# Kernel tuning notes

Hardware: AMD Instinct MI355X
Metric: run time of the kernel (lower is better)

Reference implementation:

```python
import jax, jax.numpy as jnp
import numpy as np

F = 32        # num_fields
V = 1000      # per-field vocab (field_dims[i])
D = 64        # embed_dim
B = 8192      # batch
P = F * (F - 1) // 2   # 496 pairs
IN = F * D + P          # 2544 MLP input dim
H1, H2, OUT = 1024, 512, 1000


def setup_inputs() -> dict:
    key = jax.random.key(0)
    ks = jax.random.split(key, 8)
    x = jax.random.randint(ks[0], (B, F), 0, V)
    emb_tables = jax.random.normal(ks[1], (F, V, D), dtype=jnp.float32) * 0.05
    W1 = jax.random.normal(ks[2], (IN, H1), dtype=jnp.float32) * (1.0 / np.sqrt(IN))
    b1 = jnp.zeros((H1,), dtype=jnp.float32)
    W2 = jax.random.normal(ks[3], (H1, H2), dtype=jnp.float32) * (1.0 / np.sqrt(H1))
    b2 = jnp.zeros((H2,), dtype=jnp.float32)
    W3 = jax.random.normal(ks[4], (H2, OUT), dtype=jnp.float32) * (1.0 / np.sqrt(H2))
    b3 = jnp.zeros((OUT,), dtype=jnp.float32)
    return {"x": x, "emb_tables": emb_tables, "W1": W1, "b1": b1,
            "W2": W2, "b2": b2, "W3": W3, "b3": b3}


def reference(x, emb_tables, W1, b1, W2, b2, W3, b3):
    # Per-field embedding lookup: e[b, f] = emb_tables[f, x[b, f]]  -> (B, F, D)
    e = emb_tables[jnp.arange(F)[None, :], x]
    # All pairwise inner products via one batched gram matrix, then triu gather
    gram = jnp.einsum('bid,bjd->bij', e, e)            # (B, F, F)
    iu, ju = jnp.triu_indices(F, k=1)
    cross = gram[:, iu, ju]                             # (B, P)
    h = jnp.concatenate([e.reshape(B, F * D), cross], axis=1)  # (B, IN)
    # MLP (dropout is identity in eval mode)
    h = jax.nn.relu(h @ W1 + b1)
    h = jax.nn.relu(h @ W2 + b2)
    logits = h @ W3 + b3
    return jax.nn.sigmoid(logits)
```

## Files before the change

kernel.cpp:

```cpp
#include <hip/hip_runtime.h>
#include <hip/hip_bf16.h>
#include <cmath>

#define F_   32
#define V_   1000
#define D_   64
#define B_   8192
#define IN_RAW  2544
#define IN_PAD  2560
#define H1_  1024
#define H2_  512
#define OUT_RAW 1000
#define OUT_PAD 1024

typedef __attribute__((ext_vector_type(4))) float f32x4;
typedef __attribute__((ext_vector_type(8))) __bf16 bf16x8;

typedef const __attribute__((address_space(1))) void* gptr_t;
typedef __attribute__((address_space(3))) void* lptr_t;

__device__ __forceinline__ void gload_lds16(const void* g, void* l) {
  __builtin_amdgcn_global_load_lds((gptr_t)g, (lptr_t)l, 16, 0, 0);
}

#define MF(a, b, c) __builtin_amdgcn_mfma_f32_16x16x32_bf16((a), (b), (c), 0, 0, 0)
#define SBAR asm volatile("s_barrier" ::: "memory")
#define WAITV(n) asm volatile("s_waitcnt vmcnt(" #n ")" ::: "memory")

__global__ __launch_bounds__(256)
void prep_kernel(const int* __restrict__ x, const float* __restrict__ emb,
                 const float* __restrict__ W1, const float* __restrict__ W2,
                 const float* __restrict__ W3,
                 __hip_bfloat16* __restrict__ h, __hip_bfloat16* __restrict__ w1t,
                 __hip_bfloat16* __restrict__ w2t, __hip_bfloat16* __restrict__ w3t)
{
  __shared__ __align__(16) char smem[16384];
  const int bid = blockIdx.x;
  const int tid = threadIdx.x;

  if (bid < 3584) {
    const float* W; __hip_bfloat16* Wt; int K, N, Kpad, kb, nb;
    if (bid < 2560)      { W = W1; Wt = w1t; K = IN_RAW; N = H1_;     Kpad = IN_PAD; kb = bid % 80; nb = bid / 80; }
    else if (bid < 3072) { int r = bid - 2560; W = W2; Wt = w2t; K = H1_; N = H2_;   Kpad = H1_;   kb = r % 32;  nb = r / 32; }
    else                 { int r = bid - 3072; W = W3; Wt = w3t; K = H2_; N = OUT_RAW; Kpad = H2_; kb = r % 16;  nb = r / 16; }
    float (*t)[33] = (float(*)[33])smem;
    const int k0 = kb * 32, n0 = nb * 32;
    const int tx = tid & 31, ty = tid >> 5;
#pragma unroll
    for (int i = 0; i < 4; ++i) {
      int r = ty + i * 8;
      int k = k0 + r, n = n0 + tx;
      t[r][tx] = (k < K && n < N) ? W[(size_t)k * N + n] : 0.f;
    }
    __syncthreads();
#pragma unroll
    for (int i = 0; i < 4; ++i) {
      int r = ty + i * 8;
      Wt[(size_t)(n0 + r) * Kpad + (k0 + tx)] = __float2bfloat16(t[tx][r]);
    }
  } else {
    __hip_bfloat16 (*e4)[2048] = (__hip_bfloat16(*)[2048])smem;
    const int wid  = tid >> 6;
    const int lane = tid & 63;
    const int b = (bid - 3584) * 4 + wid;
    const int* xb = x + b * F_;
    const size_t hrow = (size_t)b * IN_PAD;

#pragma unroll
    for (int it = 0; it < 8; ++it) {
      const int r = it * 4 + (lane >> 4);
      const int d = (lane & 15) * 4;
      const int idx = xb[r];
      const float4 v = *reinterpret_cast<const float4*>(
          &emb[((size_t)r * V_ + idx) * D_ + d]);
      __hip_bfloat16 tb[4];
      tb[0] = __float2bfloat16(v.x); tb[1] = __float2bfloat16(v.y);
      tb[2] = __float2bfloat16(v.z); tb[3] = __float2bfloat16(v.w);
      const ushort4 pk = *reinterpret_cast<const ushort4*>(tb);
      *reinterpret_cast<ushort4*>(&h[hrow + r * 64 + d]) = pk;
      const int ch = (d >> 3) ^ (r & 7);
      *reinterpret_cast<ushort4*>(&e4[wid][r * 64 + ch * 8 + (d & 7)]) = pk;
    }
    __syncthreads();

    f32x4 g[2][2] = {};
#pragma unroll
    for (int kk = 0; kk < 2; ++kk) {
      bf16x8 fa[2];
#pragma unroll
      for (int t2 = 0; t2 < 2; ++t2) {
        const int r = t2 * 16 + (lane & 15);
        const int ch = (kk * 4 + (lane >> 4)) ^ (r & 7);
        fa[t2] = *reinterpret_cast<const bf16x8*>(&e4[wid][r * 64 + ch * 8]);
      }
#pragma unroll
      for (int ti = 0; ti < 2; ++ti)
#pragma unroll
        for (int tj = 0; tj < 2; ++tj)
          g[ti][tj] = MF(fa[ti], fa[tj], g[ti][tj]);
    }

#pragma unroll
    for (int ti = 0; ti < 2; ++ti)
#pragma unroll
      for (int tj = 0; tj < 2; ++tj) {
        const int jj = tj * 16 + (lane & 15);
#pragma unroll
        for (int q = 0; q < 4; ++q) {
          const int i = ti * 16 + (lane >> 4) * 4 + q;
          if (i < jj) {
            const int p = i * 31 - (i * (i - 1)) / 2 + (jj - i - 1);
            h[hrow + 2048 + p] = __float2bfloat16(g[ti][tj][q]);
          }
        }
      }
    if (lane < IN_PAD - IN_RAW) h[hrow + IN_RAW + lane] = __float2bfloat16(0.f);
  }
}

template <int EPI>
__device__ __forceinline__ void gemm_body(
    const __hip_bfloat16* __restrict__ A,
    const __hip_bfloat16* __restrict__ Bt,
    const float* __restrict__ bias,
    void* __restrict__ Cout,
    int M, int N, int K, int Nreal)
{
  __shared__ __align__(16) char lds[4][32768];

  const int tid  = threadIdx.x;
  const int wid  = tid >> 6;
  const int lane = tid & 63;
  const int wr = wid >> 1, wc = wid & 1;
  const int lr = lane & 15;
  const int lhi = lane >> 4;
  const long rowBase = (long)blockIdx.x * 128;
  const long colBase = (long)blockIdx.y * 128;

  f32x4 acc[4][4] = {};

  const int prow  = tid >> 2;
  const int pch   = tid & 3;
  const int s7    = (prow >> 1) & 7;
  const int lslot = (((prow & 1) << 2) | pch) ^ s7;
  const int lrow  = ((prow >> 1) << 1) | (lslot >> 2);
  const int lch8  = (lslot & 3) << 3;
  const __hip_bfloat16* A0 = A  + (rowBase + lrow) * (long)K + lch8;
  const __hip_bfloat16* A1 = A  + (rowBase + 64 + lrow) * (long)K + lch8;
  const __hip_bfloat16* B0 = Bt + (colBase + lrow) * (long)K + lch8;
  const __hip_bfloat16* B1 = Bt + (colBase + 64 + lrow) * (long)K + lch8;
  char* const ldsw = &lds[0][0] + wid * 1024;

  const int NT = K >> 5;

  auto STAGE = [&](int buf, int t) {
    const long k0 = (long)t << 5;
    char* lb = ldsw + buf * 32768;
    gload_lds16(A0 + k0, lb);
    gload_lds16(A1 + k0, lb + 4096);
    gload_lds16(B0 + k0, lb + 16384);
    gload_lds16(B1 + k0, lb + 20480);
  };

  auto loff = [&](int r, int c) -> int {
    return ((r >> 1) << 7) + (((((r & 1) << 2) | c) ^ ((r >> 1) & 7)) << 4);
  };

  auto COMPUTE = [&](int buf) {
    const char* ba = &lds[0][0] + buf * 32768;
    const char* bb = ba + 16384;
    bf16x8 af[4], bv[4];
#pragma unroll
    for (int m = 0; m < 4; ++m)
      af[m] = *reinterpret_cast<const bf16x8*>(ba + loff(wr * 64 + m * 16 + lr, lhi));
#pragma unroll
    for (int n = 0; n < 4; ++n)
      bv[n] = *reinterpret_cast<const bf16x8*>(bb + loff(wc * 64 + n * 16 + lr, lhi));
#pragma unroll
    for (int m = 0; m < 4; ++m)
#pragma unroll
      for (int n = 0; n < 4; ++n)
        acc[m][n] = MF(af[m], bv[n], acc[m][n]);
  };

  STAGE(0, 0); STAGE(1, 1); STAGE(2, 2);
  WAITV(8); SBAR;

  for (int t = 0; t < NT; ++t) {
    if (t + 3 < NT) STAGE((t + 3) & 3, t + 3);
    COMPUTE(t & 3);
    if (t + 3 < NT)      { WAITV(8); SBAR; }
    else if (t + 2 < NT) { WAITV(4); SBAR; }
    else if (t + 1 < NT) { WAITV(0); SBAR; }
  }

#pragma unroll
  for (int m = 0; m < 4; ++m) {
    const long row0 = rowBase + wr * 64 + m * 16 + lhi * 4;
#pragma unroll
    for (int n = 0; n < 4; ++n) {
      const int col = (int)colBase + wc * 64 + n * 16 + lr;
      const float bvs = (col < Nreal) ? bias[col] : 0.f;
#pragma unroll
      for (int j = 0; j < 4; ++j) {
        float v = acc[m][n][j] + bvs;
        const long row = row0 + j;
        if (EPI == 0) {
          ((__hip_bfloat16*)Cout)[row * N + col] = __float2bfloat16(fmaxf(v, 0.f));
        } else {
          if (col < Nreal)
            ((float*)Cout)[row * Nreal + col] = 1.f / (1.f + expf(-v));
        }
      }
    }
  }
}

__global__ __launch_bounds__(256)
void gemm_L1(const __hip_bfloat16* A, const __hip_bfloat16* Bt, const float* bias,
             void* C, int M, int N, int K, int Nreal) {
  gemm_body<0>(A, Bt, bias, C, M, N, K, Nreal);
}
__global__ __launch_bounds__(256)
void gemm_L2(const __hip_bfloat16* A, const __hip_bfloat16* Bt, const float* bias,
             void* C, int M, int N, int K, int Nreal) {
  gemm_body<0>(A, Bt, bias, C, M, N, K, Nreal);
}
__global__ __launch_bounds__(256)
void gemm_L3(const __hip_bfloat16* A, const __hip_bfloat16* Bt, const float* bias,
             void* C, int M, int N, int K, int Nreal) {
  gemm_body<1>(A, Bt, bias, C, M, N, K, Nreal);
}

extern "C" void kernel_launch(void* const* d_in, const int* in_sizes, int n_in,
                              void* d_out, int out_size, void* d_ws, size_t ws_size,
                              hipStream_t stream)
{
  const int*   x   = (const int*)  d_in[0];
  const float* emb = (const float*)d_in[1];
  const float* W1  = (const float*)d_in[2];
  const float* b1  = (const float*)d_in[3];
  const float* W2  = (const float*)d_in[4];
  const float* b2  = (const float*)d_in[5];
  const float* W3  = (const float*)d_in[6];
  const float* b3  = (const float*)d_in[7];
  float* out = (float*)d_out;

  char* ws = (char*)d_ws;
  size_t off = 0;
  auto alloc = [&](size_t bytes) { size_t o = off; off = (off + bytes + 255) & ~255ULL; return o; };
  __hip_bfloat16* h   = (__hip_bfloat16*)(ws + alloc((size_t)B_ * IN_PAD * 2));
  __hip_bfloat16* w1t = (__hip_bfloat16*)(ws + alloc((size_t)H1_ * IN_PAD * 2));
  __hip_bfloat16* w2t = (__hip_bfloat16*)(ws + alloc((size_t)H2_ * H1_ * 2));
  __hip_bfloat16* w3t = (__hip_bfloat16*)(ws + alloc((size_t)OUT_PAD * H2_ * 2));
  __hip_bfloat16* h1  = (__hip_bfloat16*)(ws + alloc((size_t)B_ * H1_ * 2));
  __hip_bfloat16* h2  = (__hip_bfloat16*)(ws + alloc((size_t)B_ * H2_ * 2));

  prep_kernel<<<5632, 256, 0, stream>>>(x, emb, W1, W2, W3, h, w1t, w2t, w3t);

  gemm_L1<<<dim3(B_ / 128, H1_ / 128), 256, 0, stream>>>(h, w1t, b1, h1, B_, H1_, IN_PAD, H1_);
  gemm_L2<<<dim3(B_ / 128, H2_ / 128), 256, 0, stream>>>(h1, w2t, b2, h2, B_, H2_, H1_, H2_);
  gemm_L3<<<dim3(B_ / 128, OUT_PAD / 128), 256, 0, stream>>>(h2, w3t, b3, out, B_, OUT_PAD, H2_, OUT_RAW);
}
```

Measured before the change: 218.1 us.

## Restructure GEMM pipeline to BK=64 double buffering with XCD-swizzled 1D grid

Rewrites the shared GEMM body to stage 64-wide K tiles into two LDS buffers instead of four 32-wide buffers, with an XOR-swizzled row layout and __syncthreads in place of manual vmcnt waits. The launch becomes a 1D grid remapped so that consecutive blocks spread across the 8 XCDs for better L2 reuse, and layer 2 uses 128x64 tiles to raise the block count. The sigmoid switches to the fast __expf. Prefetch depth drops from three stages to one, so memory latency is less hidden, while the larger K step halves the number of barriers.

```diff
diff --git a/kernel.cpp b/kernel.cpp
--- a/kernel.cpp
+++ b/kernel.cpp
@@ -24,8 +24,6 @@
 }
 
 #define MF(a, b, c) __builtin_amdgcn_mfma_f32_16x16x32_bf16((a), (b), (c), 0, 0, 0)
-#define SBAR asm volatile("s_barrier" ::: "memory")
-#define WAITV(n) asm volatile("s_waitcnt vmcnt(" #n ")" ::: "memory")
 
 __global__ __launch_bounds__(256)
 void prep_kernel(const int* __restrict__ x, const float* __restrict__ emb,
@@ -118,7 +116,7 @@
   }
 }
 
-template <int EPI>
+template <int EPI, int NW>
 __device__ __forceinline__ void gemm_body(
     const __hip_bfloat16* __restrict__ A,
     const __hip_bfloat16* __restrict__ Bt,
@@ -126,7 +124,11 @@
     void* __restrict__ Cout,
     int M, int N, int K, int Nreal)
 {
-  __shared__ __align__(16) char lds[4][32768];
+  constexpr int BN = NW * 32;
+  constexpr int ABYTES = 128 * 64 * 2;
+  constexpr int BBYTES = BN * 64 * 2;
+  constexpr int BUFB = ABYTES + BBYTES;
+  __shared__ __align__(16) char lds[2][BUFB];
 
   const int tid  = threadIdx.x;
   const int wid  = tid >> 6;
@@ -134,82 +136,80 @@
   const int wr = wid >> 1, wc = wid & 1;
   const int lr = lane & 15;
   const int lhi = lane >> 4;
-  const long rowBase = (long)blockIdx.x * 128;
-  const long colBase = (long)blockIdx.y * 128;
-
-  f32x4 acc[4][4] = {};
-
-  const int prow  = tid >> 2;
-  const int pch   = tid & 3;
-  const int s7    = (prow >> 1) & 7;
-  const int lslot = (((prow & 1) << 2) | pch) ^ s7;
-  const int lrow  = ((prow >> 1) << 1) | (lslot >> 2);
-  const int lch8  = (lslot & 3) << 3;
-  const __hip_bfloat16* A0 = A  + (rowBase + lrow) * (long)K + lch8;
-  const __hip_bfloat16* A1 = A  + (rowBase + 64 + lrow) * (long)K + lch8;
-  const __hip_bfloat16* B0 = Bt + (colBase + lrow) * (long)K + lch8;
-  const __hip_bfloat16* B1 = Bt + (colBase + 64 + lrow) * (long)K + lch8;
-  char* const ldsw = &lds[0][0] + wid * 1024;
-
-  const int NT = K >> 5;
+
+  const int nCol = N / BN;
+  const int nwg  = gridDim.x;
+  const int bid  = blockIdx.x;
+  const int swz  = (bid & 7) * (nwg >> 3) + (bid >> 3);
+  const long rowBase = (long)(swz / nCol) * 128;
+  const long colBase = (long)(swz % nCol) * BN;
+
+  f32x4 acc[4][NW] = {};
+
+  const int srow = tid >> 3;
+  const long scol = (long)(((tid & 7) ^ (srow & 7)) * 8);
+  const long aBase = (rowBase + srow) * (long)K + scol;
+  const long bBase = (colBase + srow) * (long)K + scol;
+
+  const int NT = K >> 6;
 
   auto STAGE = [&](int buf, int t) {
-    const long k0 = (long)t << 5;
-    char* lb = ldsw + buf * 32768;
-    gload_lds16(A0 + k0, lb);
-    gload_lds16(A1 + k0, lb + 4096);
-    gload_lds16(B0 + k0, lb + 16384);
-    gload_lds16(B1 + k0, lb + 20480);
+    const long k0 = (long)t * 64;
+    char* la = &lds[buf][0] + wid * 1024;
+    char* lb = &lds[buf][ABYTES] + wid * 1024;
+#pragma unroll
+    for (int j = 0; j < 4; ++j)
+      gload_lds16(A + aBase + (long)j * 32 * K + k0, la + j * 4096);
+#pragma unroll
+    for (int j = 0; j < BN / 32; ++j)
+      gload_lds16(Bt + bBase + (long)j * 32 * K + k0, lb + j * 4096);
   };
 
-  auto loff = [&](int r, int c) -> int {
-    return ((r >> 1) << 7) + (((((r & 1) << 2) | c) ^ ((r >> 1) & 7)) << 4);
-  };
-
-  auto COMPUTE = [&](int buf) {
-    const char* ba = &lds[0][0] + buf * 32768;
-    const char* bb = ba + 16384;
-    bf16x8 af[4], bv[4];
-#pragma unroll
-    for (int m = 0; m < 4; ++m)
-      af[m] = *reinterpret_cast<const bf16x8*>(ba + loff(wr * 64 + m * 16 + lr, lhi));
-#pragma unroll
-    for (int n = 0; n < 4; ++n)
-      bv[n] = *reinterpret_cast<const bf16x8*>(bb + loff(wc * 64 + n * 16 + lr, lhi));
-#pragma unroll
-    for (int m = 0; m < 4; ++m)
-#pragma unroll
-      for (int n = 0; n < 4; ++n)
-        acc[m][n] = MF(af[m], bv[n], acc[m][n]);
-  };
-
-  STAGE(0, 0); STAGE(1, 1); STAGE(2, 2);
-  WAITV(8); SBAR;
-
+  STAGE(0, 0);
+  __syncthreads();
+
+  int cur = 0;
   for (int t = 0; t < NT; ++t) {
-    if (t + 3 < NT) STAGE((t + 3) & 3, t + 3);
-    COMPUTE(t & 3);
-    if (t + 3 < NT)      { WAITV(8); SBAR; }
-    else if (t + 2 < NT) { WAITV(4); SBAR; }
-    else if (t + 1 < NT) { WAITV(0); SBAR; }
+    if (t + 1 < NT) STAGE(cur ^ 1, t + 1);
+
+    const __hip_bfloat16* la = (const __hip_bfloat16*)&lds[cur][0];
+    const __hip_bfloat16* lb = (const __hip_bfloat16*)&lds[cur][ABYTES];
+#pragma unroll
+    for (int kk = 0; kk < 2; ++kk) {
+      const int ch = ((kk * 4 + lhi) ^ (lane & 7)) * 8;
+      bf16x8 af[4], bfv[NW];
+#pragma unroll
+      for (int m = 0; m < 4; ++m)
+        af[m] = *reinterpret_cast<const bf16x8*>(&la[(wr * 64 + m * 16 + lr) * 64 + ch]);
+#pragma unroll
+      for (int n = 0; n < NW; ++n)
+        bfv[n] = *reinterpret_cast<const bf16x8*>(&lb[(wc * (BN / 2) + n * 16 + lr) * 64 + ch]);
+#pragma unroll
+      for (int m = 0; m < 4; ++m)
+#pragma unroll
+        for (int n = 0; n < NW; ++n)
+          acc[m][n] = MF(af[m], bfv[n], acc[m][n]);
+    }
+    __syncthreads();
+    cur ^= 1;
   }
 
 #pragma unroll
   for (int m = 0; m < 4; ++m) {
     const long row0 = rowBase + wr * 64 + m * 16 + lhi * 4;
 #pragma unroll
-    for (int n = 0; n < 4; ++n) {
-      const int col = (int)colBase + wc * 64 + n * 16 + lr;
-      const float bvs = (col < Nreal) ? bias[col] : 0.f;
+    for (int n = 0; n < NW; ++n) {
+      const int col = (int)colBase + wc * (BN / 2) + n * 16 + lr;
+      const float bv = (col < Nreal) ? bias[col] : 0.f;
 #pragma unroll
       for (int j = 0; j < 4; ++j) {
-        float v = acc[m][n][j] + bvs;
+        float v = acc[m][n][j] + bv;
         const long row = row0 + j;
         if (EPI == 0) {
           ((__hip_bfloat16*)Cout)[row * N + col] = __float2bfloat16(fmaxf(v, 0.f));
         } else {
           if (col < Nreal)
-            ((float*)Cout)[row * Nreal + col] = 1.f / (1.f + expf(-v));
+            ((float*)Cout)[row * Nreal + col] = 1.f / (1.f + __expf(-v));
         }
       }
     }
@@ -219,17 +219,17 @@
 __global__ __launch_bounds__(256)
 void gemm_L1(const __hip_bfloat16* A, const __hip_bfloat16* Bt, const float* bias,
              void* C, int M, int N, int K, int Nreal) {
-  gemm_body<0>(A, Bt, bias, C, M, N, K, Nreal);
+  gemm_body<0, 4>(A, Bt, bias, C, M, N, K, Nreal);
 }
 __global__ __launch_bounds__(256)
 void gemm_L2(const __hip_bfloat16* A, const __hip_bfloat16* Bt, const float* bias,
              void* C, int M, int N, int K, int Nreal) {
-  gemm_body<0>(A, Bt, bias, C, M, N, K, Nreal);
+  gemm_body<0, 2>(A, Bt, bias, C, M, N, K, Nreal);
 }
 __global__ __launch_bounds__(256)
 void gemm_L3(const __hip_bfloat16* A, const __hip_bfloat16* Bt, const float* bias,
              void* C, int M, int N, int K, int Nreal) {
-  gemm_body<1>(A, Bt, bias, C, M, N, K, Nreal);
+  gemm_body<1, 4>(A, Bt, bias, C, M, N, K, Nreal);
 }
 
 extern "C" void kernel_launch(void* const* d_in, const int* in_sizes, int n_in,
@@ -258,7 +258,7 @@
 
   prep_kernel<<<5632, 256, 0, stream>>>(x, emb, W1, W2, W3, h, w1t, w2t, w3t);
 
-  gemm_L1<<<dim3(B_ / 128, H1_ / 128), 256, 0, stream>>>(h, w1t, b1, h1, B_, H1_, IN_PAD, H1_);
-  gemm_L2<<<dim3(B_ / 128, H2_ / 128), 256, 0, stream>>>(h1, w2t, b2, h2, B_, H2_, H1_, H2_);
-  gemm_L3<<<dim3(B_ / 128, OUT_PAD / 128), 256, 0, stream>>>(h2, w3t, b3, out, B_, OUT_PAD, H2_, OUT_RAW);
-}
+  gemm_L1<<<(B_ / 128) * (H1_ / 128), 256, 0, stream>>>(h, w1t, b1, h1, B_, H1_, IN_PAD, H1_);
+  gemm_L2<<<(B_ / 128) * (H2_ / 64), 256, 0, stream>>>(h1, w2t, b2, h2, B_, H2_, H1_, H2_);
+  gemm_L3<<<(B_ / 128) * (OUT_PAD / 128), 256, 0, stream>>>(h2, w3t, b3, out, B_, OUT_PAD, H2_, OUT_RAW);
+}
```

New measurement: 182.8 us. 16.2% less time.
